# Optimization experiments

Measured on AMD Instinct MI355X. Metric: run time of the kernel, lower is better.

## Reference

```python
import jax, jax.numpy as jnp
import numpy as np

DIM = 1024
DEPTH = 4
HEADS = 16
MLP = 4096
B, N = 4, 1024
SCALE = DIM ** (-0.5)  # NOTE: module scales by dim^-0.5, not head_dim^-0.5
EPS = 1e-5


def setup_inputs() -> dict:
    key = jax.random.key(0)
    ks = jax.random.split(key, 13)
    s = 0.02
    return {
        "x": jax.random.normal(ks[0], (B, N, DIM), dtype=jnp.float32),
        "ln1_g": jnp.ones((DEPTH, DIM), jnp.float32),
        "ln1_b": jnp.zeros((DEPTH, DIM), jnp.float32),
        "w_qkv": jax.random.normal(ks[1], (DEPTH, DIM, 3 * DIM), jnp.float32) * s,
        "w_out": jax.random.normal(ks[2], (DEPTH, DIM, DIM), jnp.float32) * s,
        "b_out": jnp.zeros((DEPTH, DIM), jnp.float32),
        "ln2_g": jnp.ones((DEPTH, DIM), jnp.float32),
        "ln2_b": jnp.zeros((DEPTH, DIM), jnp.float32),
        "w1": jax.random.normal(ks[3], (DEPTH, DIM, MLP), jnp.float32) * s,
        "b1": jnp.zeros((DEPTH, MLP), jnp.float32),
        "w2": jax.random.normal(ks[4], (DEPTH, MLP, DIM), jnp.float32) * s,
        "b2": jnp.zeros((DEPTH, DIM), jnp.float32),
    }


def _layernorm(x, g, b):
    m = jnp.mean(x, axis=-1, keepdims=True)
    v = jnp.mean(jnp.square(x - m), axis=-1, keepdims=True)
    return (x - m) * jax.lax.rsqrt(v + EPS) * g + b


def _gelu(x):
    # x * 0.5 * (1 + erf(x / sqrt(2)))  (exact GeLu from the module)
    return x * 0.5 * (1.0 + jax.lax.erf(x / jnp.sqrt(2.0).astype(x.dtype)))


def _block(x, p):
    ln1_g, ln1_b, w_qkv, w_out, b_out, ln2_g, ln2_b, w1, b1, w2, b2 = p
    # --- attention (pre-norm, residual) ---
    h = _layernorm(x, ln1_g, ln1_b)
    qkv = h @ w_qkv  # [b, n, 3*dim]
    q, k, v = jnp.split(qkv, 3, axis=-1)
    def heads(t):  # [b, n, dim] -> [b, h, n, d]
        b_, n_, _ = t.shape
        return t.reshape(b_, n_, HEADS, DIM // HEADS).transpose(0, 2, 1, 3)
    q, k, v = heads(q), heads(k), heads(v)
    dots = jnp.einsum('bhid,bhjd->bhij', q, k) * SCALE
    attn = jax.nn.softmax(dots, axis=-1)
    o = jnp.einsum('bhij,bhjd->bhid', attn, v)
    o = o.transpose(0, 2, 1, 3).reshape(x.shape)  # [b, n, dim]
    x = x + (o @ w_out + b_out)
    # --- feed-forward (pre-norm, residual) ---
    h = _layernorm(x, ln2_g, ln2_b)
    x = x + (_gelu(h @ w1 + b1) @ w2 + b2)
    return x


def reference(x, ln1_g, ln1_b, w_qkv, w_out, b_out, ln2_g, ln2_b, w1, b1, w2, b2):
    for l in range(DEPTH):
        p = (ln1_g[l], ln1_b[l], w_qkv[l], w_out[l], b_out[l],
             ln2_g[l], ln2_b[l], w1[l], b1[l], w2[l], b2[l])
        x = _block(x, p)
    return x
```

## Files before the change

### kernel.cpp

```cpp
#include <hip/hip_runtime.h>

typedef __bf16 bf16;
typedef __bf16 bf16x4 __attribute__((ext_vector_type(4)));
typedef __bf16 bf16x8 __attribute__((ext_vector_type(8)));
typedef float  f32x4  __attribute__((ext_vector_type(4)));

#define DIMV   1024
#define MLPV   4096
#define MROWS  4096
#define NHEAD  16
#define SCALEV 0.03125f
#define QKV_LD 3072
#define MB (1024ull * 1024ull)

__device__ __forceinline__ void gload16(const bf16* g, bf16* l) {
    __builtin_amdgcn_global_load_lds((const __attribute__((address_space(1))) unsigned int*)g,
                                     (__attribute__((address_space(3))) unsigned int*)l,
                                     16, 0, 0);
}

__global__ __launch_bounds__(256) void k_ln(const float* __restrict__ x,
                                            const float* __restrict__ g,
                                            const float* __restrict__ b,
                                            bf16* __restrict__ h) {
    int row = blockIdx.x;
    int tid = threadIdx.x;
    const f32x4 v = ((const f32x4*)(x + (size_t)row * DIMV))[tid];
    float s  = v[0]+v[1]+v[2]+v[3];
    float sq = v[0]*v[0]+v[1]*v[1]+v[2]*v[2]+v[3]*v[3];
    for (int m = 1; m < 64; m <<= 1) { s += __shfl_xor(s, m, 64); sq += __shfl_xor(sq, m, 64); }
    __shared__ float ss[4], ssq[4];
    int w = tid >> 6, lane = tid & 63;
    if (lane == 0) { ss[w] = s; ssq[w] = sq; }
    __syncthreads();
    s  = ss[0]+ss[1]+ss[2]+ss[3];
    sq = ssq[0]+ssq[1]+ssq[2]+ssq[3];
    float mean = s * (1.f/DIMV);
    float var  = sq * (1.f/DIMV) - mean*mean;
    float rs   = rsqrtf(var + 1e-5f);
    int c0 = tid * 4;
    const f32x4 gv = ((const f32x4*)(g))[tid];
    const f32x4 bv = ((const f32x4*)(b))[tid];
    bf16x4 o;
    for (int i = 0; i < 4; i++)
        o[i] = (bf16)((v[i]-mean)*rs*gv[i] + bv[i]);
    *(bf16x4*)(h + (size_t)row * DIMV + c0) = o;
}

__global__ __launch_bounds__(256) void k_transpose_cvt(const float* __restrict__ in,
                                                       bf16* __restrict__ out, int R, int C) {
    __shared__ float tile[32][33];
    int tx = threadIdx.x & 31, ty = threadIdx.x >> 5;
    int r0 = blockIdx.y * 32, c0 = blockIdx.x * 32;
    for (int i = 0; i < 4; i++)
        tile[ty + 8*i][tx] = in[(size_t)(r0 + ty + 8*i) * C + c0 + tx];
    __syncthreads();
    for (int i = 0; i < 4; i++)
        out[(size_t)(c0 + ty + 8*i) * R + r0 + tx] = (bf16)tile[tx][ty + 8*i];
}

__global__ __launch_bounds__(256) void k_vt(const bf16* __restrict__ big, bf16* __restrict__ vT) {
    __shared__ bf16 tile[32][33];
    int tx = threadIdx.x & 31, ty = threadIdx.x >> 5;
    int hd0 = blockIdx.x * 32, s0 = blockIdx.y * 32, bb = blockIdx.z;
    const bf16* src = big + (size_t)bb * 1024 * QKV_LD + 2048;
    for (int i = 0; i < 4; i++)
        tile[ty + 8*i][tx] = src[(size_t)(s0 + ty + 8*i) * QKV_LD + hd0 + tx];
    __syncthreads();
    bf16* dst = vT + (size_t)bb * 1024 * 1024;
    for (int i = 0; i < 4; i++)
        dst[(size_t)(hd0 + ty + 8*i) * 1024 + s0 + tx] = tile[tx][ty + 8*i];
}

template<int EPI, int TN>
__global__ __launch_bounds__(256) void k_gemm(const bf16* __restrict__ A,
                                              const bf16* __restrict__ Bt,
                                              const float* __restrict__ bias,
                                              bf16* __restrict__ Cb,
                                              float* __restrict__ Cacc,
                                              int N, int K) {
    constexpr int NWN = TN / 64;
    constexpr int MT  = (TN == 128) ? 4 : 2;
    __shared__ alignas(16) bf16 As[2][128 * 64];
    __shared__ alignas(16) bf16 Bs[2][TN * 64];
    const int tid  = threadIdx.x;
    const int lane = tid & 63, w = tid >> 6;
    const int quad = lane >> 4, l16 = lane & 15;
    const int wm = w / NWN, wn = w % NWN;

    const int gx   = (int)gridDim.x;
    const int nwg  = gx * (int)gridDim.y;
    const int orig = (int)blockIdx.y * gx + (int)blockIdx.x;
    const int qq = nwg >> 3, rr = nwg & 7;
    const int xcd = orig & 7, loc = orig >> 3;
    const int wg  = (xcd < rr ? xcd * (qq + 1) : rr * (qq + 1) + (xcd - rr) * qq) + loc;
    const int bn = wg % gx, bm = wg / gx;

    const bf16* Ag = A  + (size_t)bm * 128 * K;
    const bf16* Bg = Bt + (size_t)bn * TN * K;

    const int srow = lane >> 3;
    const int scol = lane & 7;
    const int sswz = (scol ^ srow) << 3;

    f32x4 acc[MT][4];
    f32x4 zero = {0.f,0.f,0.f,0.f};
    for (int mt = 0; mt < MT; mt++) for (int nt = 0; nt < 4; nt++) acc[mt][nt] = zero;

    auto stage = [&](int p, int k0) {
        #pragma unroll
        for (int i = 0; i < 4; i++) {
            int row = w * 32 + i * 8;
            gload16(&Ag[(size_t)(row + srow) * K + k0 + sswz], &As[p][row * 64]);
        }
        #pragma unroll
        for (int i = 0; i < TN / 32; i++) {
            int row = w * (TN / 4) + i * 8;
            gload16(&Bg[(size_t)(row + srow) * K + k0 + sswz], &Bs[p][row * 64]);
        }
    };

    const int NT = K >> 6;
    stage(0, 0);
    __syncthreads();

    for (int t = 0; t < NT; t++) {
        const int p = t & 1;
        if (t + 1 < NT) stage(p ^ 1, (t + 1) << 6);

        bf16x8 af[MT][2], bfr[4][2];
        #pragma unroll
        for (int mt = 0; mt < MT; mt++)
            #pragma unroll
            for (int ks = 0; ks < 2; ks++) {
                int row = wm * (MT * 16) + mt * 16 + l16;
                int kb  = ks * 4 + quad;
                af[mt][ks] = *(const bf16x8*)&As[p][row * 64 + ((kb ^ (row & 7)) << 3)];
            }
        #pragma unroll
        for (int nt = 0; nt < 4; nt++)
            #pragma unroll
            for (int ks = 0; ks < 2; ks++) {
                int row = wn * 64 + nt * 16 + l16;
                int kb  = ks * 4 + quad;
                bfr[nt][ks] = *(const bf16x8*)&Bs[p][row * 64 + ((kb ^ (row & 7)) << 3)];
            }
        #pragma unroll
        for (int ks = 0; ks < 2; ks++)
            #pragma unroll
            for (int mt = 0; mt < MT; mt++)
                #pragma unroll
                for (int nt = 0; nt < 4; nt++)
                    acc[mt][nt] = __builtin_amdgcn_mfma_f32_16x16x32_bf16(af[mt][ks], bfr[nt][ks], acc[mt][nt], 0, 0, 0);

        __syncthreads();
    }

    for (int mt = 0; mt < MT; mt++) for (int nt = 0; nt < 4; nt++) {
        int col = bn * TN + wn * 64 + nt * 16 + l16;
        float bval = (EPI >= 1) ? bias[col] : 0.f;
        for (int r = 0; r < 4; r++) {
            int row = bm * 128 + wm * (MT * 16) + mt * 16 + quad * 4 + r;
            float v = acc[mt][nt][r];
            if (EPI == 0) {
                Cb[(size_t)row * N + col] = (bf16)v;
            } else if (EPI == 1) {
                float t = v + bval;
                float ge = 0.5f * t * (1.f + erff(t * 0.70710678118f));
                Cb[(size_t)row * N + col] = (bf16)ge;
            } else {
                Cacc[(size_t)row * N + col] += v + bval;
            }
        }
    }
}

__global__ __launch_bounds__(256) void k_attn(const bf16* __restrict__ qkv,
                                              const bf16* __restrict__ vT,
                                              bf16* __restrict__ o) {
    const int qt = blockIdx.x;
    const int h  = blockIdx.y;
    const int bb = blockIdx.z;
    const int tid  = threadIdx.x;
    const int lane = tid & 63, w = tid >> 6;
    const int quad = lane >> 4, l16 = lane & 15;
    const int srow = lane >> 3, scol = lane & 7;
    const int sswz = (scol ^ srow) << 3;

    __shared__ alignas(16) bf16 Qs[128 * 64];
    __shared__ alignas(16) bf16 Ks[2][64 * 64];
    __shared__ alignas(16) bf16 Vs[2][64 * 64];
    __shared__ alignas(16) bf16 Ps[128 * 72];

    const bf16* qbase  = qkv + (size_t)(bb*1024 + qt*128) * QKV_LD + h*64;
    const bf16* kbase0 = qkv + (size_t)(bb*1024) * QKV_LD + 1024 + h*64;
    const bf16* vbase0 = vT  + ((size_t)bb*1024 + h*64) * 1024;

    #pragma unroll
    for (int i = 0; i < 4; i++) {
        int row = w * 32 + i * 8;
        gload16(&qbase[(size_t)(row + srow) * QKV_LD + sswz], &Qs[row * 64]);
    }
    auto stageKV = [&](int p, int kt) {
        #pragma unroll
        for (int i = 0; i < 2; i++) {
            int row = w * 16 + i * 8;
            gload16(&kbase0[(size_t)(kt*64 + row + srow) * QKV_LD + sswz], &Ks[p][row * 64]);
            gload16(&vbase0[(size_t)(row + srow) * 1024 + kt*64 + sswz],   &Vs[p][row * 64]);
        }
    };

    f32x4 o_acc[2][4];
    f32x4 zero = {0.f,0.f,0.f,0.f};
    for (int mt = 0; mt < 2; mt++) for (int nt = 0; nt < 4; nt++) o_acc[mt][nt] = zero;
    float l_st[2][4];
    for (int mt = 0; mt < 2; mt++) for (int r = 0; r < 4; r++) l_st[mt][r] = 0.f;

    stageKV(0, 0);
    __syncthreads();

    for (int kt = 0; kt < 16; kt++) {
        const int p = kt & 1;
        if (kt < 15) stageKV(p ^ 1, kt + 1);

        f32x4 sv[2][4];
        __builtin_amdgcn_s_setprio(1);
        for (int mt = 0; mt < 2; mt++) for (int nt = 0; nt < 4; nt++) {
            f32x4 a = zero;
            #pragma unroll
            for (int ks = 0; ks < 2; ks++) {
                int kb = ks * 4 + quad;
                bf16x8 qf = *(const bf16x8*)&Qs[(w*32 + mt*16 + l16) * 64 + ((kb ^ (l16 & 7)) << 3)];
                bf16x8 kf = *(const bf16x8*)&Ks[p][(nt*16 + l16) * 64 + ((kb ^ (l16 & 7)) << 3)];
                a = __builtin_amdgcn_mfma_f32_16x16x32_bf16(qf, kf, a, 0, 0, 0);
            }
            sv[mt][nt] = a;
        }
        __builtin_amdgcn_s_setprio(0);

        for (int mt = 0; mt < 2; mt++) for (int r = 0; r < 4; r++) {
            float rs = 0.f;
            for (int nt = 0; nt < 4; nt++) {
                float pe = __expf(sv[mt][nt][r] * SCALEV);
                sv[mt][nt][r] = pe;
                rs += pe;
            }
            for (int msk = 1; msk < 16; msk <<= 1) rs += __shfl_xor(rs, msk, 64);
            l_st[mt][r] += rs;
        }

        for (int mt = 0; mt < 2; mt++) for (int nt = 0; nt < 4; nt++)
            for (int r = 0; r < 4; r++)
                Ps[(w*32 + mt*16 + quad*4 + r) * 72 + nt*16 + l16] = (bf16)sv[mt][nt][r];
        asm volatile("s_waitcnt lgkmcnt(0)" ::: "memory");
        __builtin_amdgcn_sched_barrier(0);

        __builtin_amdgcn_s_setprio(1);
        for (int mt = 0; mt < 2; mt++) for (int nt = 0; nt < 4; nt++) {
            f32x4 a = o_acc[mt][nt];
            #pragma unroll
            for (int ks = 0; ks < 2; ks++) {
                int kb = ks * 4 + quad;
                bf16x8 pf = *(const bf16x8*)&Ps[(w*32 + mt*16 + l16) * 72 + ks*32 + quad*8];
                bf16x8 vf = *(const bf16x8*)&Vs[p][(nt*16 + l16) * 64 + ((kb ^ (l16 & 7)) << 3)];
                a = __builtin_amdgcn_mfma_f32_16x16x32_bf16(pf, vf, a, 0, 0, 0);
            }
            o_acc[mt][nt] = a;
        }
        __builtin_amdgcn_s_setprio(0);

        __syncthreads();
    }

    for (int mt = 0; mt < 2; mt++) for (int nt = 0; nt < 4; nt++)
        for (int r = 0; r < 4; r++) {
            float val = o_acc[mt][nt][r] / l_st[mt][r];
            int row = qt*128 + w*32 + mt*16 + quad*4 + r;
            o[(size_t)(bb*1024 + row) * DIMV + h*64 + nt*16 + l16] = (bf16)val;
        }
}

extern "C" void kernel_launch(void* const* d_in, const int* in_sizes, int n_in,
                              void* d_out, int out_size, void* d_ws, size_t ws_size,
                              hipStream_t stream) {
    (void)in_sizes; (void)n_in; (void)out_size;
    const float* x_in  = (const float*)d_in[0];
    const float* ln1_g = (const float*)d_in[1];
    const float* ln1_b = (const float*)d_in[2];
    const float* w_qkv = (const float*)d_in[3];
    const float* w_out = (const float*)d_in[4];
    const float* b_out = (const float*)d_in[5];
    const float* ln2_g = (const float*)d_in[6];
    const float* ln2_b = (const float*)d_in[7];
    const float* w1    = (const float*)d_in[8];
    const float* b1    = (const float*)d_in[9];
    const float* w2    = (const float*)d_in[10];
    const float* b2    = (const float*)d_in[11];

    char* ws = (char*)d_ws;
    float* xf32    = (float*)ws;
    bf16*  h       = (bf16*)(ws + 16*MB);
    bf16*  wT1     = (bf16*)(ws + 24*MB);
    bf16*  wT2     = (bf16*)(ws + 32*MB);
    bf16*  attn_o  = (bf16*)(ws + 40*MB);
    bf16*  big     = (bf16*)(ws + 48*MB);
    size_t bigsz   = (ws_size > 48*MB) ? (ws_size - 48*MB) : 0;

    int G = 4;
    while (G > 1 && (size_t)G * 8*MB > bigsz) G >>= 1;
    int RC = 4096;
    while (RC > 128 && (size_t)RC * 8192ull > bigsz) RC >>= 1;

    bf16* vT = big + (size_t)G * 1024 * QKV_LD;

    hipMemcpyAsync(xf32, x_in, (size_t)MROWS * DIMV * sizeof(float),
                   hipMemcpyDeviceToDevice, stream);

    for (int l = 0; l < 4; l++) {
        k_ln<<<MROWS, 256, 0, stream>>>(xf32, ln1_g + (size_t)l*DIMV, ln1_b + (size_t)l*DIMV, h);
        k_transpose_cvt<<<dim3(3072/32, 1024/32), 256, 0, stream>>>(w_qkv + (size_t)l*DIMV*3072, wT1, 1024, 3072);
        for (int g = 0; g < 4; g += G) {
            k_gemm<0,128><<<dim3(3072/128, (G*1024)/128), 256, 0, stream>>>(
                h + (size_t)g*1024*DIMV, wT1, (const float*)nullptr, big, (float*)nullptr, 3072, 1024);
            k_vt<<<dim3(32, 32, G), 256, 0, stream>>>(big, vT);
            k_attn<<<dim3(8, NHEAD, G), 256, 0, stream>>>(big, vT, attn_o + (size_t)g*1024*DIMV);
        }
        k_transpose_cvt<<<dim3(1024/32, 1024/32), 256, 0, stream>>>(w_out + (size_t)l*DIMV*DIMV, wT1, 1024, 1024);
        k_gemm<2,64><<<dim3(1024/64, 4096/128), 256, 0, stream>>>(
            attn_o, wT1, b_out + (size_t)l*DIMV, (bf16*)nullptr, xf32, 1024, 1024);

        k_ln<<<MROWS, 256, 0, stream>>>(xf32, ln2_g + (size_t)l*DIMV, ln2_b + (size_t)l*DIMV, h);
        k_transpose_cvt<<<dim3(4096/32, 1024/32), 256, 0, stream>>>(w1 + (size_t)l*DIMV*MLPV, wT1, 1024, 4096);
        k_transpose_cvt<<<dim3(1024/32, 4096/32), 256, 0, stream>>>(w2 + (size_t)l*MLPV*DIMV, wT2, 4096, 1024);
        for (int r0 = 0; r0 < 4096; r0 += RC) {
            k_gemm<1,128><<<dim3(4096/128, RC/128), 256, 0, stream>>>(
                h + (size_t)r0*DIMV, wT1, b1 + (size_t)l*MLPV, big, (float*)nullptr, 4096, 1024);
            k_gemm<2,64><<<dim3(1024/64, RC/128), 256, 0, stream>>>(
                big, wT2, b2 + (size_t)l*DIMV, (bf16*)nullptr, xf32 + (size_t)r0*DIMV, 1024, 4096);
        }
    }

    hipMemcpyAsync(d_out, xf32, (size_t)MROWS * DIMV * sizeof(float),
                   hipMemcpyDeviceToDevice, stream);
}
```

Before: 1.233 ms.

## Triple-buffer GEMM loads with explicit vmcnt waits and unify to 128x64 tiles

```diff
diff --git a/kernel.cpp b/kernel.cpp
--- a/kernel.cpp
+++ b/kernel.cpp
@@ -18,6 +18,10 @@
                                      (__attribute__((address_space(3))) unsigned int*)l,
                                      16, 0, 0);
 }
+__device__ __forceinline__ void sb0()        { __builtin_amdgcn_sched_barrier(0); }
+__device__ __forceinline__ void wait_vm6()   { asm volatile("s_waitcnt vmcnt(6)" ::: "memory"); }
+__device__ __forceinline__ void wait_vm0()   { asm volatile("s_waitcnt vmcnt(0)" ::: "memory"); }
+__device__ __forceinline__ void wait_lgkm0() { asm volatile("s_waitcnt lgkmcnt(0)" ::: "memory"); }
 
 __global__ __launch_bounds__(256) void k_ln(const float* __restrict__ x,
                                             const float* __restrict__ g,
@@ -72,21 +76,18 @@
         dst[(size_t)(hd0 + ty + 8*i) * 1024 + s0 + tx] = tile[tx][ty + 8*i];
 }
 
-template<int EPI, int TN>
+template<int EPI>
 __global__ __launch_bounds__(256) void k_gemm(const bf16* __restrict__ A,
                                               const bf16* __restrict__ Bt,
                                               const float* __restrict__ bias,
                                               bf16* __restrict__ Cb,
                                               float* __restrict__ Cacc,
                                               int N, int K) {
-    constexpr int NWN = TN / 64;
-    constexpr int MT  = (TN == 128) ? 4 : 2;
-    __shared__ alignas(16) bf16 As[2][128 * 64];
-    __shared__ alignas(16) bf16 Bs[2][TN * 64];
+    __shared__ alignas(16) bf16 As[3][128 * 64];
+    __shared__ alignas(16) bf16 Bs[3][64 * 64];
     const int tid  = threadIdx.x;
     const int lane = tid & 63, w = tid >> 6;
     const int quad = lane >> 4, l16 = lane & 15;
-    const int wm = w / NWN, wn = w % NWN;
 
     const int gx   = (int)gridDim.x;
     const int nwg  = gx * (int)gridDim.y;
@@ -97,43 +98,48 @@
     const int bn = wg % gx, bm = wg / gx;
 
     const bf16* Ag = A  + (size_t)bm * 128 * K;
-    const bf16* Bg = Bt + (size_t)bn * TN * K;
+    const bf16* Bg = Bt + (size_t)bn * 64 * K;
 
     const int srow = lane >> 3;
     const int scol = lane & 7;
     const int sswz = (scol ^ srow) << 3;
 
-    f32x4 acc[MT][4];
+    f32x4 acc[2][4];
     f32x4 zero = {0.f,0.f,0.f,0.f};
-    for (int mt = 0; mt < MT; mt++) for (int nt = 0; nt < 4; nt++) acc[mt][nt] = zero;
-
-    auto stage = [&](int p, int k0) {
+    for (int mt = 0; mt < 2; mt++) for (int nt = 0; nt < 4; nt++) acc[mt][nt] = zero;
+
+    auto stage = [&](int p, int t) {
+        int k0 = t << 6;
         #pragma unroll
         for (int i = 0; i < 4; i++) {
             int row = w * 32 + i * 8;
             gload16(&Ag[(size_t)(row + srow) * K + k0 + sswz], &As[p][row * 64]);
         }
         #pragma unroll
-        for (int i = 0; i < TN / 32; i++) {
-            int row = w * (TN / 4) + i * 8;
+        for (int i = 0; i < 2; i++) {
+            int row = w * 16 + i * 8;
             gload16(&Bg[(size_t)(row + srow) * K + k0 + sswz], &Bs[p][row * 64]);
         }
     };
 
     const int NT = K >> 6;
     stage(0, 0);
-    __syncthreads();
+    stage(1, 1);
+    wait_vm6();
+    sb0(); __builtin_amdgcn_s_barrier(); sb0();
 
     for (int t = 0; t < NT; t++) {
-        const int p = t & 1;
-        if (t + 1 < NT) stage(p ^ 1, (t + 1) << 6);
-
-        bf16x8 af[MT][2], bfr[4][2];
-        #pragma unroll
-        for (int mt = 0; mt < MT; mt++)
+        const int p = t % 3;
+        const bool more = (t + 2 < NT);
+        if (more) stage((t + 2) % 3, t + 2);
+        sb0();
+
+        bf16x8 af[2][2], bfr[4][2];
+        #pragma unroll
+        for (int mt = 0; mt < 2; mt++)
             #pragma unroll
             for (int ks = 0; ks < 2; ks++) {
-                int row = wm * (MT * 16) + mt * 16 + l16;
+                int row = w * 32 + mt * 16 + l16;
                 int kb  = ks * 4 + quad;
                 af[mt][ks] = *(const bf16x8*)&As[p][row * 64 + ((kb ^ (row & 7)) << 3)];
             }
@@ -141,26 +147,32 @@
         for (int nt = 0; nt < 4; nt++)
             #pragma unroll
             for (int ks = 0; ks < 2; ks++) {
-                int row = wn * 64 + nt * 16 + l16;
+                int row = nt * 16 + l16;
                 int kb  = ks * 4 + quad;
                 bfr[nt][ks] = *(const bf16x8*)&Bs[p][row * 64 + ((kb ^ (row & 7)) << 3)];
             }
+        __builtin_amdgcn_s_setprio(1);
         #pragma unroll
         for (int ks = 0; ks < 2; ks++)
             #pragma unroll
-            for (int mt = 0; mt < MT; mt++)
+            for (int mt = 0; mt < 2; mt++)
                 #pragma unroll
                 for (int nt = 0; nt < 4; nt++)
                     acc[mt][nt] = __builtin_amdgcn_mfma_f32_16x16x32_bf16(af[mt][ks], bfr[nt][ks], acc[mt][nt], 0, 0, 0);
-
-        __syncthreads();
-    }
-
-    for (int mt = 0; mt < MT; mt++) for (int nt = 0; nt < 4; nt++) {
-        int col = bn * TN + wn * 64 + nt * 16 + l16;
+        __builtin_amdgcn_s_setprio(0);
+
+        sb0();
+        wait_lgkm0();
+        if (more) wait_vm6();
+        else      wait_vm0();
+        sb0(); __builtin_amdgcn_s_barrier(); sb0();
+    }
+
+    for (int mt = 0; mt < 2; mt++) for (int nt = 0; nt < 4; nt++) {
+        int col = bn * 64 + nt * 16 + l16;
         float bval = (EPI >= 1) ? bias[col] : 0.f;
         for (int r = 0; r < 4; r++) {
-            int row = bm * 128 + wm * (MT * 16) + mt * 16 + quad * 4 + r;
+            int row = bm * 128 + w * 32 + mt * 16 + quad * 4 + r;
             float v = acc[mt][nt][r];
             if (EPI == 0) {
                 Cb[(size_t)row * N + col] = (bf16)v;
@@ -320,22 +332,22 @@
         k_ln<<<MROWS, 256, 0, stream>>>(xf32, ln1_g + (size_t)l*DIMV, ln1_b + (size_t)l*DIMV, h);
         k_transpose_cvt<<<dim3(3072/32, 1024/32), 256, 0, stream>>>(w_qkv + (size_t)l*DIMV*3072, wT1, 1024, 3072);
         for (int g = 0; g < 4; g += G) {
-            k_gemm<0,128><<<dim3(3072/128, (G*1024)/128), 256, 0, stream>>>(
+            k_gemm<0><<<dim3(3072/64, (G*1024)/128), 256, 0, stream>>>(
                 h + (size_t)g*1024*DIMV, wT1, (const float*)nullptr, big, (float*)nullptr, 3072, 1024);
             k_vt<<<dim3(32, 32, G), 256, 0, stream>>>(big, vT);
             k_attn<<<dim3(8, NHEAD, G), 256, 0, stream>>>(big, vT, attn_o + (size_t)g*1024*DIMV);
         }
         k_transpose_cvt<<<dim3(1024/32, 1024/32), 256, 0, stream>>>(w_out + (size_t)l*DIMV*DIMV, wT1, 1024, 1024);
-        k_gemm<2,64><<<dim3(1024/64, 4096/128), 256, 0, stream>>>(
+        k_gemm<2><<<dim3(1024/64, 4096/128), 256, 0, stream>>>(
             attn_o, wT1, b_out + (size_t)l*DIMV, (bf16*)nullptr, xf32, 1024, 1024);
 
         k_ln<<<MROWS, 256, 0, stream>>>(xf32, ln2_g + (size_t)l*DIMV, ln2_b + (size_t)l*DIMV, h);
         k_transpose_cvt<<<dim3(4096/32, 1024/32), 256, 0, stream>>>(w1 + (size_t)l*DIMV*MLPV, wT1, 1024, 4096);
         k_transpose_cvt<<<dim3(1024/32, 4096/32), 256, 0, stream>>>(w2 + (size_t)l*MLPV*DIMV, wT2, 4096, 1024);
         for (int r0 = 0; r0 < 4096; r0 += RC) {
-            k_gemm<1,128><<<dim3(4096/128, RC/128), 256, 0, stream>>>(
+            k_gemm<1><<<dim3(4096/64, RC/128), 256, 0, stream>>>(
                 h + (size_t)r0*DIMV, wT1, b1 + (size_t)l*MLPV, big, (float*)nullptr, 4096, 1024);
-            k_gemm<2,64><<<dim3(1024/64, RC/128), 256, 0, stream>>>(
+            k_gemm<2><<<dim3(1024/64, RC/128), 256, 0, stream>>>(
                 big, wT2, b2 + (size_t)l*DIMV, (bf16*)nullptr, xf32 + (size_t)r0*DIMV, 1024, 4096);
         }
     }
```

Result: slower. 1.388 ms (+12.6%).

## Split-K the MLP down-projection and fold the partial sum into the next LayerNorm

Applied to the files above, without the earlier changes.

```diff
diff --git a/kernel.cpp b/kernel.cpp
--- a/kernel.cpp
+++ b/kernel.cpp
@@ -45,6 +45,45 @@
     for (int i = 0; i < 4; i++)
         o[i] = (bf16)((v[i]-mean)*rs*gv[i] + bv[i]);
     *(bf16x4*)(h + (size_t)row * DIMV + c0) = o;
+}
+
+__global__ __launch_bounds__(256) void k_lnr(float* __restrict__ x,
+                                             const float* __restrict__ g,
+                                             const float* __restrict__ b,
+                                             const float* __restrict__ P1,
+                                             bf16* __restrict__ h) {
+    int row = blockIdx.x;
+    int tid = threadIdx.x;
+    f32x4 v = ((const f32x4*)(x  + (size_t)row * DIMV))[tid];
+    const f32x4 p = ((const f32x4*)(P1 + (size_t)row * DIMV))[tid];
+    for (int i = 0; i < 4; i++) v[i] += p[i];
+    ((f32x4*)(x + (size_t)row * DIMV))[tid] = v;
+    float s  = v[0]+v[1]+v[2]+v[3];
+    float sq = v[0]*v[0]+v[1]*v[1]+v[2]*v[2]+v[3]*v[3];
+    for (int m = 1; m < 64; m <<= 1) { s += __shfl_xor(s, m, 64); sq += __shfl_xor(sq, m, 64); }
+    __shared__ float ss[4], ssq[4];
+    int w = tid >> 6, lane = tid & 63;
+    if (lane == 0) { ss[w] = s; ssq[w] = sq; }
+    __syncthreads();
+    s  = ss[0]+ss[1]+ss[2]+ss[3];
+    sq = ssq[0]+ssq[1]+ssq[2]+ssq[3];
+    float mean = s * (1.f/DIMV);
+    float var  = sq * (1.f/DIMV) - mean*mean;
+    float rs   = rsqrtf(var + 1e-5f);
+    const f32x4 gv = ((const f32x4*)(g))[tid];
+    const f32x4 bv = ((const f32x4*)(b))[tid];
+    bf16x4 o;
+    for (int i = 0; i < 4; i++)
+        o[i] = (bf16)((v[i]-mean)*rs*gv[i] + bv[i]);
+    *(bf16x4*)(h + (size_t)row * DIMV + tid*4) = o;
+}
+
+__global__ __launch_bounds__(256) void k_fin(float* __restrict__ x, const float* __restrict__ P1) {
+    size_t i = (size_t)blockIdx.x * 1024 + threadIdx.x * 4;
+    f32x4 v = *(const f32x4*)(x + i);
+    const f32x4 p = *(const f32x4*)(P1 + i);
+    for (int k = 0; k < 4; k++) v[k] += p[k];
+    *(f32x4*)(x + i) = v;
 }
 
 __global__ __launch_bounds__(256) void k_transpose_cvt(const float* __restrict__ in,
@@ -96,6 +135,11 @@
     const int wg  = (xcd < rr ? xcd * (qq + 1) : rr * (qq + 1) + (xcd - rr) * qq) + loc;
     const int bn = wg % gx, bm = wg / gx;
 
+    const int KZ  = (int)gridDim.z;
+    const int kz  = (int)blockIdx.z;
+    const int Kc  = K / KZ;
+    const int tk0 = (kz * Kc) >> 6;
+
     const bf16* Ag = A  + (size_t)bm * 128 * K;
     const bf16* Bg = Bt + (size_t)bn * TN * K;
 
@@ -120,13 +164,13 @@
         }
     };
 
-    const int NT = K >> 6;
-    stage(0, 0);
+    const int NT = Kc >> 6;
+    stage(0, tk0 << 6);
     __syncthreads();
 
     for (int t = 0; t < NT; t++) {
         const int p = t & 1;
-        if (t + 1 < NT) stage(p ^ 1, (t + 1) << 6);
+        if (t + 1 < NT) stage(p ^ 1, (tk0 + t + 1) << 6);
 
         bf16x8 af[MT][2], bfr[4][2];
         #pragma unroll
@@ -168,8 +212,11 @@
                 float t = v + bval;
                 float ge = 0.5f * t * (1.f + erff(t * 0.70710678118f));
                 Cb[(size_t)row * N + col] = (bf16)ge;
+            } else if (EPI == 2) {
+                Cacc[(size_t)row * N + col] += v + bval;
             } else {
-                Cacc[(size_t)row * N + col] += v + bval;
+                if (kz == 0) Cacc[(size_t)row * N + col] += v + bval;
+                else         ((float*)Cb)[(size_t)row * N + col] = v;
             }
         }
     }
@@ -311,13 +358,18 @@
     int RC = 4096;
     while (RC > 128 && (size_t)RC * 8192ull > bigsz) RC >>= 1;
 
-    bf16* vT = big + (size_t)G * 1024 * QKV_LD;
+    bf16*  vT = big + (size_t)G * 1024 * QKV_LD;
+    const bool useP = (bigsz >= 48*MB) && (RC == 4096);
+    float* P1 = (float*)((char*)big + 32*MB);
 
     hipMemcpyAsync(xf32, x_in, (size_t)MROWS * DIMV * sizeof(float),
                    hipMemcpyDeviceToDevice, stream);
 
     for (int l = 0; l < 4; l++) {
-        k_ln<<<MROWS, 256, 0, stream>>>(xf32, ln1_g + (size_t)l*DIMV, ln1_b + (size_t)l*DIMV, h);
+        if (l > 0 && useP)
+            k_lnr<<<MROWS, 256, 0, stream>>>(xf32, ln1_g + (size_t)l*DIMV, ln1_b + (size_t)l*DIMV, P1, h);
+        else
+            k_ln<<<MROWS, 256, 0, stream>>>(xf32, ln1_g + (size_t)l*DIMV, ln1_b + (size_t)l*DIMV, h);
         k_transpose_cvt<<<dim3(3072/32, 1024/32), 256, 0, stream>>>(w_qkv + (size_t)l*DIMV*3072, wT1, 1024, 3072);
         for (int g = 0; g < 4; g += G) {
             k_gemm<0,128><<<dim3(3072/128, (G*1024)/128), 256, 0, stream>>>(
@@ -335,10 +387,17 @@
         for (int r0 = 0; r0 < 4096; r0 += RC) {
             k_gemm<1,128><<<dim3(4096/128, RC/128), 256, 0, stream>>>(
                 h + (size_t)r0*DIMV, wT1, b1 + (size_t)l*MLPV, big, (float*)nullptr, 4096, 1024);
-            k_gemm<2,64><<<dim3(1024/64, RC/128), 256, 0, stream>>>(
-                big, wT2, b2 + (size_t)l*DIMV, (bf16*)nullptr, xf32 + (size_t)r0*DIMV, 1024, 4096);
+            if (useP) {
+                k_gemm<3,128><<<dim3(1024/128, RC/128, 2), 256, 0, stream>>>(
+                    big, wT2, b2 + (size_t)l*DIMV, (bf16*)(P1 + (size_t)r0*DIMV),
+                    xf32 + (size_t)r0*DIMV, 1024, 4096);
+            } else {
+                k_gemm<2,64><<<dim3(1024/64, RC/128), 256, 0, stream>>>(
+                    big, wT2, b2 + (size_t)l*DIMV, (bf16*)nullptr, xf32 + (size_t)r0*DIMV, 1024, 4096);
+            }
         }
     }
+    if (useP) k_fin<<<MROWS, 256, 0, stream>>>(xf32, P1);
 
     hipMemcpyAsync(d_out, xf32, (size_t)MROWS * DIMV * sizeof(float),
                    hipMemcpyDeviceToDevice, stream);
```

Result: no change. 1.228 ms (-0.4%).
